# Kernel optimization log

Hardware: AMD Instinct MI355X
Metric: run time of the kernel (lower is better)

Reference implementation:

```python
import jax, jax.numpy as jnp
import numpy as np

H = 16          # num heads
DH = 64         # head size
D = H * DH      # hidden size 1024
B, S = 2, 2048


def setup_inputs() -> dict:
    key = jax.random.key(0)
    ks = jax.random.split(key, 9)
    scale = 1.0 / np.sqrt(D)
    p = {}
    p["hidden_states"] = jax.random.normal(ks[0], (B, S, D), dtype=jnp.float32)
    for i, name in enumerate(["q", "k", "v", "o"]):
        # stored so that y = x @ W + b (transpose of torch Linear weight)
        p[f"W{name}"] = jax.random.normal(ks[1 + 2 * i], (D, D), dtype=jnp.float32) * scale
        p[f"b{name}"] = jax.random.normal(ks[2 + 2 * i], (D,), dtype=jnp.float32) * 0.01
    return p


def reference(hidden_states, Wq, bq, Wk, bk, Wv, bv, Wo, bo):
    b, s, _ = hidden_states.shape
    q = hidden_states @ Wq + bq  # [B,S,D]
    k = hidden_states @ Wk + bk
    v = hidden_states @ Wv + bv
    # [B,H,S,DH]
    q = q.reshape(b, s, H, DH).transpose(0, 2, 1, 3)
    k = k.reshape(b, s, H, DH).transpose(0, 2, 1, 3)
    v = v.reshape(b, s, H, DH).transpose(0, 2, 1, 3)
    scores = jnp.einsum("bhqd,bhkd->bhqk", q, k) / np.sqrt(DH)
    causal = jnp.triu(jnp.ones((s, s), dtype=bool), k=1)  # True above diagonal -> masked
    scores = jnp.where(causal, -jnp.inf, scores)
    attn = jax.nn.softmax(scores, axis=-1)  # dropout p=0 (eval)
    ctx = jnp.einsum("bhqk,bhkd->bhqd", attn, v)
    ctx = ctx.transpose(0, 2, 1, 3).reshape(b, s, D)
    return ctx @ Wo + bo
```

## Files before the change

kernel.cpp:

```cpp
#include <hip/hip_runtime.h>


typedef _Float16 f16x8 __attribute__((ext_vector_type(8)));
typedef _Float16 f16x4 __attribute__((ext_vector_type(4)));
typedef float f32x4 __attribute__((ext_vector_type(4)));

#define GLD_LDS16(g, l)                                                        \
  __builtin_amdgcn_global_load_lds(                                            \
      (__attribute__((address_space(1))) const unsigned int*)(g),              \
      (__attribute__((address_space(3))) unsigned int*)(l), 16, 0, 0)

static constexpr int Sdim = 2048;
static constexpr int Ddim = 1024;
static constexpr int NH = 16;
static constexpr int DH = 64;
static constexpr int Mrows = 4096;

static constexpr float QSCALE = 0.125f * 1.44269504f;
static constexpr float SHIFT = 4.0f;

__global__ __launch_bounds__(256) void xcvt(const float* __restrict__ X,
                                            _Float16* __restrict__ Y) {
  size_t i = ((size_t)blockIdx.x * 256 + threadIdx.x) * 8;
  float4 f0 = *(const float4*)(X + i);
  float4 f1 = *(const float4*)(X + i + 4);
  alignas(16) _Float16 h[8] = {(_Float16)f0.x, (_Float16)f0.y, (_Float16)f0.z,
                               (_Float16)f0.w, (_Float16)f1.x, (_Float16)f1.y,
                               (_Float16)f1.z, (_Float16)f1.w};
  *(uint4*)(Y + i) = *(const uint4*)h;
}

struct WtArgs {
  const float *s0, *s1, *s2, *s3;
  _Float16 *d0, *d1, *d2, *d3;
};

__global__ __launch_bounds__(256) void wtrans(WtArgs a) {
  __shared__ _Float16 L[64 * 72];
  const int z = blockIdx.z;
  const float* src = z == 0 ? a.s0 : z == 1 ? a.s1 : z == 2 ? a.s2 : a.s3;
  _Float16* dst = z == 0 ? a.d0 : z == 1 ? a.d1 : z == 2 ? a.d2 : a.d3;
  const int k0 = blockIdx.x * 64, n0 = blockIdx.y * 64, t = threadIdx.x;
#pragma unroll
  for (int i = 0; i < 4; ++i) {
    int c = i * 256 + t;
    int row = c >> 4, cc = c & 15;
    float4 f = *(const float4*)&src[(size_t)(k0 + row) * Ddim + n0 + cc * 4];
    L[(cc * 4 + 0) * 72 + row] = (_Float16)f.x;
    L[(cc * 4 + 1) * 72 + row] = (_Float16)f.y;
    L[(cc * 4 + 2) * 72 + row] = (_Float16)f.z;
    L[(cc * 4 + 3) * 72 + row] = (_Float16)f.w;
  }
  __syncthreads();
#pragma unroll
  for (int i = 0; i < 2; ++i) {
    int c = i * 256 + t;
    int n = c >> 3, cc = c & 7;
    *(uint4*)&dst[(size_t)(n0 + n) * Ddim + k0 + cc * 8] =
        *(const uint4*)&L[n * 72 + cc * 8];
  }
}

struct GemmArgs {
  const _Float16* A;
  const _Float16 *Bt0, *Bt1, *Bt2;
  const float *b0, *b1, *b2;
  void *o0, *o1, *o2;
};

template <int MODE>
__global__ __launch_bounds__(256) void gemm128(GemmArgs g) {
  constexpr int K = 1024;
  __shared__ _Float16 As[128 * 32];
  __shared__ _Float16 Bs[128 * 32];
  const int z = blockIdx.z;
  const _Float16* A = g.A;
  const _Float16* Bt = z == 0 ? g.Bt0 : z == 1 ? g.Bt1 : g.Bt2;
  const float* bias = z == 0 ? g.b0 : z == 1 ? g.b1 : g.b2;
  void* out = z == 0 ? g.o0 : z == 1 ? g.o1 : g.o2;
  const int m0 = blockIdx.x * 128, n0 = blockIdx.y * 128;
  const int t = threadIdx.x, lane = t & 63, wv = t >> 6;
  const int wm = wv >> 1, wn = wv & 1, quad = lane >> 4, r = lane & 15;

  const int c0 = wv * 64 + lane, c1 = c0 + 256;
  const _Float16* ga0 = A + (size_t)(m0 + (c0 >> 2)) * K + (c0 & 3) * 8;
  const _Float16* ga1 = A + (size_t)(m0 + (c1 >> 2)) * K + (c1 & 3) * 8;
  const _Float16* gb0 = Bt + (size_t)(n0 + (c0 >> 2)) * K + (c0 & 3) * 8;
  const _Float16* gb1 = Bt + (size_t)(n0 + (c1 >> 2)) * K + (c1 & 3) * 8;
  char* lA0 = (char*)As + (wv * 64) * 16;
  char* lA1 = (char*)As + (256 + wv * 64) * 16;
  char* lB0 = (char*)Bs + (wv * 64) * 16;
  char* lB1 = (char*)Bs + (256 + wv * 64) * 16;

  f32x4 acc[4][4] = {};
  for (int kt = 0; kt < K; kt += 32) {
    GLD_LDS16(ga0 + kt, lA0);
    GLD_LDS16(ga1 + kt, lA1);
    GLD_LDS16(gb0 + kt, lB0);
    GLD_LDS16(gb1 + kt, lB1);
    __syncthreads();
    f16x8 af[4], bf[4];
#pragma unroll
    for (int mi = 0; mi < 4; ++mi)
      af[mi] = *(const f16x8*)&As[(wm * 64 + mi * 16 + r) * 32 + quad * 8];
#pragma unroll
    for (int ni = 0; ni < 4; ++ni)
      bf[ni] = *(const f16x8*)&Bs[(wn * 64 + ni * 16 + r) * 32 + quad * 8];
#pragma unroll
    for (int mi = 0; mi < 4; ++mi)
#pragma unroll
      for (int ni = 0; ni < 4; ++ni)
        acc[mi][ni] = __builtin_amdgcn_mfma_f32_16x16x32_f16(af[mi], bf[ni],
                                                             acc[mi][ni], 0, 0, 0);
    __syncthreads();
  }

  const float scale = (MODE == 0 && z == 0) ? QSCALE : 1.0f;
  float bv[4];
#pragma unroll
  for (int ni = 0; ni < 4; ++ni) bv[ni] = bias[n0 + wn * 64 + ni * 16 + r];
#pragma unroll
  for (int mi = 0; mi < 4; ++mi) {
#pragma unroll
    for (int ni = 0; ni < 4; ++ni) {
      const int n = n0 + wn * 64 + ni * 16 + r;
      if (MODE == 0 && z == 2) {
        alignas(8) _Float16 h4[4];
#pragma unroll
        for (int reg = 0; reg < 4; ++reg)
          h4[reg] = (_Float16)(acc[mi][ni][reg] + bv[ni]);
        const int m = m0 + wm * 64 + mi * 16 + quad * 4;
        const int b = m >> 11, s = m & 2047, h = n >> 6, dh = n & 63;
        *(uint2*)&((_Float16*)out)[((size_t)(b * NH + h) * DH + dh) * Sdim + s] =
            *(const uint2*)h4;
      } else {
#pragma unroll
        for (int reg = 0; reg < 4; ++reg) {
          const int m = m0 + wm * 64 + mi * 16 + quad * 4 + reg;
          const float v = (acc[mi][ni][reg] + bv[ni]) * scale;
          if (MODE == 0) {
            const int b = m >> 11, s = m & 2047, h = n >> 6, dh = n & 63;
            ((_Float16*)out)[(((size_t)(b * NH + h) * Sdim + s) << 6) + dh] =
                (_Float16)v;
          } else {
            ((float*)out)[(size_t)m * Ddim + n] = v;
          }
        }
      }
    }
  }
}

__global__ __launch_bounds__(256) void attn(const _Float16* __restrict__ Q,
                                            const _Float16* __restrict__ Kk,
                                            const _Float16* __restrict__ Vt,
                                            _Float16* __restrict__ ctx) {
  constexpr int LDK = 72;
  __shared__ _Float16 Ks[2][64 * LDK], Vs[2][64 * LDK], Ps[4 * 16 * LDK];
  const int id = blockIdx.x, xcd = id & 7, slot = id >> 3;
  const int x = slot & 15, bh = ((slot >> 4) << 3) | xcd;
  const int t = threadIdx.x, lane = t & 63, wv = t >> 6;
  const int quad = lane >> 4, r = lane & 15;
  const _Float16* Kg = Kk + (size_t)bh * Sdim * DH;
  const _Float16* Vg = Vt + (size_t)bh * DH * Sdim;
  _Float16* Pw = Ps + wv * 16 * LDK;
  const int b = bh >> 4, h = bh & 15;
  const int sr0 = t >> 3, sc0 = (t & 7) * 8, sr1 = (t + 256) >> 3;

#pragma unroll
  for (int pass = 0; pass < 2; ++pass) {
    const int qt = pass == 0 ? x : 31 - x;
    const int q0 = qt * 64;
    const _Float16* Qrow = Q + ((size_t)bh * Sdim + q0 + wv * 16 + r) * DH;
    const f16x8 aq0 = *(const f16x8*)(Qrow + quad * 8);
    const f16x8 aq1 = *(const f16x8*)(Qrow + 32 + quad * 8);
    const int qcol = q0 + wv * 16 + r;

    float l_i = 0.f;
    f32x4 oacc[4] = {};

    const int ntiles = qt + 1;
    uint4 ka = *(const uint4*)&Kg[(size_t)sr0 * DH + sc0];
    uint4 kb = *(const uint4*)&Kg[(size_t)sr1 * DH + sc0];
    uint4 va = *(const uint4*)&Vg[(size_t)sr0 * Sdim + sc0];
    uint4 vb = *(const uint4*)&Vg[(size_t)sr1 * Sdim + sc0];
    __syncthreads();
    *(uint4*)&Ks[0][sr0 * LDK + sc0] = ka;
    *(uint4*)&Ks[0][sr1 * LDK + sc0] = kb;
    *(uint4*)&Vs[0][sr0 * LDK + sc0] = va;
    *(uint4*)&Vs[0][sr1 * LDK + sc0] = vb;

    for (int it = 0; it < ntiles; ++it) {
      const int cur = it & 1;
      if (it + 1 < ntiles) {
        const int kvn = (it + 1) * 64;
        ka = *(const uint4*)&Kg[(size_t)(kvn + sr0) * DH + sc0];
        kb = *(const uint4*)&Kg[(size_t)(kvn + sr1) * DH + sc0];
        va = *(const uint4*)&Vg[(size_t)sr0 * Sdim + kvn + sc0];
        vb = *(const uint4*)&Vg[(size_t)sr1 * Sdim + kvn + sc0];
      }
      __syncthreads();

      f32x4 sacc[4] = {};
#pragma unroll
      for (int ks = 0; ks < 2; ++ks) {
        const f16x8 bq = ks ? aq1 : aq0;
#pragma unroll
        for (int ni = 0; ni < 4; ++ni) {
          f16x8 ak =
              *(const f16x8*)&Ks[cur][(ni * 16 + r) * LDK + ks * 32 + quad * 8];
          sacc[ni] =
              __builtin_amdgcn_mfma_f32_16x16x32_f16(ak, bq, sacc[ni], 0, 0, 0);
        }
      }

      const bool diag = (it == ntiles - 1);
      const int kvb = it * 64;
      float lp = 0.f;
#pragma unroll
      for (int ni = 0; ni < 4; ++ni) {
        alignas(8) f16x4 h4;
#pragma unroll
        for (int reg = 0; reg < 4; ++reg) {
          float sv = sacc[ni][reg];
          if (diag && (kvb + ni * 16 + quad * 4 + reg > qcol)) sv = -1e30f;
          const float p = exp2f(sv - SHIFT);
          lp += p;
          h4[reg] = (_Float16)p;
        }
        *(f16x4*)&Pw[r * LDK + ni * 16 + quad * 4] = h4;
      }
      lp += __shfl_xor(lp, 16, 64);
      lp += __shfl_xor(lp, 32, 64);
      l_i += lp;

#pragma unroll
      for (int ks = 0; ks < 2; ++ks) {
        f16x8 ap = *(const f16x8*)&Pw[r * LDK + ks * 32 + quad * 8];
#pragma unroll
        for (int ni = 0; ni < 4; ++ni) {
          f16x8 bv =
              *(const f16x8*)&Vs[cur][(ni * 16 + r) * LDK + ks * 32 + quad * 8];
          oacc[ni] =
              __builtin_amdgcn_mfma_f32_16x16x32_f16(ap, bv, oacc[ni], 0, 0, 0);
        }
      }

      if (it + 1 < ntiles) {
        const int nxt = cur ^ 1;
        *(uint4*)&Ks[nxt][sr0 * LDK + sc0] = ka;
        *(uint4*)&Ks[nxt][sr1 * LDK + sc0] = kb;
        *(uint4*)&Vs[nxt][sr0 * LDK + sc0] = va;
        *(uint4*)&Vs[nxt][sr1 * LDK + sc0] = vb;
      }
    }

#pragma unroll
    for (int reg = 0; reg < 4; ++reg) {
      const float lq = __shfl(l_i, quad * 4 + reg, 16);
      const float rl = 1.0f / lq;
      const int qrow = q0 + wv * 16 + quad * 4 + reg;
#pragma unroll
      for (int ni = 0; ni < 4; ++ni) {
        ctx[((size_t)b * Sdim + qrow) * Ddim + h * DH + ni * 16 + r] =
            (_Float16)(oacc[ni][reg] * rl);
      }
    }
  }
}

extern "C" void kernel_launch(void* const* d_in, const int* in_sizes, int n_in,
                              void* d_out, int out_size, void* d_ws,
                              size_t ws_size, hipStream_t stream) {
  const float* hid = (const float*)d_in[0];
  const float* Wq = (const float*)d_in[1];
  const float* bq = (const float*)d_in[2];
  const float* Wk = (const float*)d_in[3];
  const float* bk = (const float*)d_in[4];
  const float* Wv = (const float*)d_in[5];
  const float* bv = (const float*)d_in[6];
  const float* Wo = (const float*)d_in[7];
  const float* bo = (const float*)d_in[8];

  char* ws = (char*)d_ws;
  _Float16* Xh = (_Float16*)(ws);
  _Float16* Wqt = (_Float16*)(ws + (8ull << 20));
  _Float16* Wkt = (_Float16*)(ws + (10ull << 20));
  _Float16* Wvt = (_Float16*)(ws + (12ull << 20));
  _Float16* Wot = (_Float16*)(ws + (14ull << 20));
  _Float16* Qb = (_Float16*)(ws + (16ull << 20));
  _Float16* Kb = (_Float16*)(ws + (24ull << 20));
  _Float16* Vtb = (_Float16*)(ws + (32ull << 20));
  _Float16* ctx = Xh;

  xcvt<<<dim3(Mrows * Ddim / (256 * 8)), 256, 0, stream>>>(hid, Xh);

  WtArgs wa{Wq, Wk, Wv, Wo, Wqt, Wkt, Wvt, Wot};
  wtrans<<<dim3(16, 16, 4), 256, 0, stream>>>(wa);

  GemmArgs g1{Xh, Wqt, Wkt, Wvt, bq, bk, bv, Qb, Kb, Vtb};
  gemm128<0><<<dim3(Mrows / 128, Ddim / 128, 3), 256, 0, stream>>>(g1);

  attn<<<dim3(512), 256, 0, stream>>>(Qb, Kb, Vtb, ctx);

  GemmArgs g2{ctx, Wot, Wot, Wot, bo, bo, bo, d_out, d_out, d_out};
  gemm128<1><<<dim3(Mrows / 128, Ddim / 128, 1), 256, 0, stream>>>(g2);
}
```

Measured before the change: 193.6 us.

## Merge prep kernels, split attention into one q-tile per block with register-shuffled P

Fuses the fp16 conversion of the activations and the weight transposes into one launch, removing a kernel launch. The attention kernel now runs one query tile per block (1024 blocks instead of 512 blocks doing paired tiles) with a rebalanced tile-to-block mapping. P is passed to the PV MFMA through cross-lane shuffles in registers instead of an LDS round trip, with a transposed accumulator that allows packed output stores. The risks are extra shuffle instructions and losing the paired-tile load balancing within a block.

After: 216.2 us. 1.12x slower.

```diff
diff --git a/kernel.cpp b/kernel.cpp
--- a/kernel.cpp
+++ b/kernel.cpp
@@ -2,7 +2,6 @@
 
 
 typedef _Float16 f16x8 __attribute__((ext_vector_type(8)));
-typedef _Float16 f16x4 __attribute__((ext_vector_type(4)));
 typedef float f32x4 __attribute__((ext_vector_type(4)));
 
 #define GLD_LDS16(g, l)                                                        \
@@ -19,28 +18,29 @@
 static constexpr float QSCALE = 0.125f * 1.44269504f;
 static constexpr float SHIFT = 4.0f;
 
-__global__ __launch_bounds__(256) void xcvt(const float* __restrict__ X,
-                                            _Float16* __restrict__ Y) {
-  size_t i = ((size_t)blockIdx.x * 256 + threadIdx.x) * 8;
-  float4 f0 = *(const float4*)(X + i);
-  float4 f1 = *(const float4*)(X + i + 4);
-  alignas(16) _Float16 h[8] = {(_Float16)f0.x, (_Float16)f0.y, (_Float16)f0.z,
-                               (_Float16)f0.w, (_Float16)f1.x, (_Float16)f1.y,
-                               (_Float16)f1.z, (_Float16)f1.w};
-  *(uint4*)(Y + i) = *(const uint4*)h;
-}
-
 struct WtArgs {
   const float *s0, *s1, *s2, *s3;
   _Float16 *d0, *d1, *d2, *d3;
 };
 
-__global__ __launch_bounds__(256) void wtrans(WtArgs a) {
+__global__ __launch_bounds__(256) void prep(const float* __restrict__ X,
+                                            _Float16* __restrict__ Y, WtArgs a) {
   __shared__ _Float16 L[64 * 72];
-  const int z = blockIdx.z;
+  const int bid = blockIdx.x, t = threadIdx.x;
+  if (bid < 2048) {
+    size_t i = ((size_t)bid * 256 + t) * 8;
+    float4 f0 = *(const float4*)(X + i);
+    float4 f1 = *(const float4*)(X + i + 4);
+    alignas(16) _Float16 h[8] = {(_Float16)f0.x, (_Float16)f0.y, (_Float16)f0.z,
+                                 (_Float16)f0.w, (_Float16)f1.x, (_Float16)f1.y,
+                                 (_Float16)f1.z, (_Float16)f1.w};
+    *(uint4*)(Y + i) = *(const uint4*)h;
+    return;
+  }
+  const int w = bid - 2048, z = w >> 8, rem = w & 255;
   const float* src = z == 0 ? a.s0 : z == 1 ? a.s1 : z == 2 ? a.s2 : a.s3;
   _Float16* dst = z == 0 ? a.d0 : z == 1 ? a.d1 : z == 2 ? a.d2 : a.d3;
-  const int k0 = blockIdx.x * 64, n0 = blockIdx.y * 64, t = threadIdx.x;
+  const int k0 = (rem & 15) * 64, n0 = (rem >> 4) * 64;
 #pragma unroll
   for (int i = 0; i < 4; ++i) {
     int c = i * 256 + t;
@@ -156,116 +156,125 @@
                                             const _Float16* __restrict__ Vt,
                                             _Float16* __restrict__ ctx) {
   constexpr int LDK = 72;
-  __shared__ _Float16 Ks[2][64 * LDK], Vs[2][64 * LDK], Ps[4 * 16 * LDK];
-  const int id = blockIdx.x, xcd = id & 7, slot = id >> 3;
-  const int x = slot & 15, bh = ((slot >> 4) << 3) | xcd;
+  __shared__ _Float16 Ks[2][64 * LDK], Vs[2][64 * LDK];
+  const int id = blockIdx.x, xcd = id & 7, k = id >> 3;
+  const int b2 = (k >> 5) & 3, qi = k & 31;
+  const int gg = ((qi >> 1) + 9 * b2) & 15;
+  const int qt = (qi & 1) ? (31 - gg) : gg;
+  const int bh = xcd + 8 * b2;
   const int t = threadIdx.x, lane = t & 63, wv = t >> 6;
   const int quad = lane >> 4, r = lane & 15;
   const _Float16* Kg = Kk + (size_t)bh * Sdim * DH;
   const _Float16* Vg = Vt + (size_t)bh * DH * Sdim;
-  _Float16* Pw = Ps + wv * 16 * LDK;
+  const int q0 = qt * 64;
+
+  const _Float16* Qrow = Q + ((size_t)bh * Sdim + q0 + wv * 16 + r) * DH;
+  const f16x8 bq0 = *(const f16x8*)(Qrow + quad * 8);
+  const f16x8 bq1 = *(const f16x8*)(Qrow + 32 + quad * 8);
+
+  const int sr0 = t >> 3, sr1 = sr0 + 32, sc0 = (t & 7) * 8;
+  const _Float16* pk0 = Kg + sr0 * DH + sc0;
+  const _Float16* pk1 = Kg + sr1 * DH + sc0;
+  const _Float16* pv0 = Vg + (size_t)sr0 * Sdim + sc0;
+  const _Float16* pv1 = Vg + (size_t)sr1 * Sdim + sc0;
+
+  const int sl = ((quad & 1) << 5) + r, sh = sl + 16;
+
+  float l_i = 0.f;
+  f32x4 oaccT[4] = {};
+
+  const int ntiles = qt + 1;
+  uint4 ka = *(const uint4*)pk0, kb = *(const uint4*)pk1;
+  uint4 va = *(const uint4*)pv0, vb = *(const uint4*)pv1;
+
+  for (int it = 0; it < ntiles; ++it) {
+    const int cur = it & 1;
+    *(uint4*)&Ks[cur][sr0 * LDK + sc0] = ka;
+    *(uint4*)&Ks[cur][sr1 * LDK + sc0] = kb;
+    *(uint4*)&Vs[cur][sr0 * LDK + sc0] = va;
+    *(uint4*)&Vs[cur][sr1 * LDK + sc0] = vb;
+    __syncthreads();
+    if (it + 1 < ntiles) {
+      pk0 += 64 * DH; pk1 += 64 * DH; pv0 += 64; pv1 += 64;
+      ka = *(const uint4*)pk0; kb = *(const uint4*)pk1;
+      va = *(const uint4*)pv0; vb = *(const uint4*)pv1;
+    }
+
+    f32x4 sacc[4] = {};
+#pragma unroll
+    for (int ks = 0; ks < 2; ++ks) {
+      const f16x8 bq = ks ? bq1 : bq0;
+#pragma unroll
+      for (int ni = 0; ni < 4; ++ni) {
+        f16x8 ak =
+            *(const f16x8*)&Ks[cur][(ni * 16 + r) * LDK + ks * 32 + quad * 8];
+        sacc[ni] =
+            __builtin_amdgcn_mfma_f32_16x16x32_f16(ak, bq, sacc[ni], 0, 0, 0);
+      }
+    }
+
+    if (it == ntiles - 1) {
+      const int qloc = wv * 16 + r;
+#pragma unroll
+      for (int ni = 0; ni < 4; ++ni)
+#pragma unroll
+        for (int reg = 0; reg < 4; ++reg)
+          if (16 * ni + 4 * quad + reg > qloc) sacc[ni][reg] = -1e30f;
+    }
+    int P4x[4], P4y[4];
+    float lp = 0.f;
+#pragma unroll
+    for (int ni = 0; ni < 4; ++ni) {
+      const float p0 = exp2f(sacc[ni][0] - SHIFT);
+      const float p1 = exp2f(sacc[ni][1] - SHIFT);
+      const float p2 = exp2f(sacc[ni][2] - SHIFT);
+      const float p3 = exp2f(sacc[ni][3] - SHIFT);
+      lp += (p0 + p1) + (p2 + p3);
+      P4x[ni] = __builtin_bit_cast(int, __builtin_amdgcn_cvt_pkrtz(p0, p1));
+      P4y[ni] = __builtin_bit_cast(int, __builtin_amdgcn_cvt_pkrtz(p2, p3));
+    }
+    lp += __shfl_xor(lp, 16, 64);
+    lp += __shfl_xor(lp, 32, 64);
+    l_i += lp;
+
+#pragma unroll
+    for (int ks = 0; ks < 2; ++ks) {
+      const int ax = __shfl(P4x[2 * ks], sl, 64);
+      const int ay = __shfl(P4y[2 * ks], sl, 64);
+      const int bx = __shfl(P4x[2 * ks + 1], sl, 64);
+      const int by = __shfl(P4y[2 * ks + 1], sl, 64);
+      const int cx = __shfl(P4x[2 * ks], sh, 64);
+      const int cy = __shfl(P4y[2 * ks], sh, 64);
+      const int dx = __shfl(P4x[2 * ks + 1], sh, 64);
+      const int dy = __shfl(P4y[2 * ks + 1], sh, 64);
+      int4 bi;
+      bi.x = quad >= 2 ? bx : ax;
+      bi.y = quad >= 2 ? by : ay;
+      bi.z = quad >= 2 ? dx : cx;
+      bi.w = quad >= 2 ? dy : cy;
+      const f16x8 bp = __builtin_bit_cast(f16x8, bi);
+#pragma unroll
+      for (int ni = 0; ni < 4; ++ni) {
+        f16x8 av =
+            *(const f16x8*)&Vs[cur][(ni * 16 + r) * LDK + ks * 32 + quad * 8];
+        oaccT[ni] =
+            __builtin_amdgcn_mfma_f32_16x16x32_f16(av, bp, oaccT[ni], 0, 0, 0);
+      }
+    }
+  }
+
   const int b = bh >> 4, h = bh & 15;
-  const int sr0 = t >> 3, sc0 = (t & 7) * 8, sr1 = (t + 256) >> 3;
-
-#pragma unroll
-  for (int pass = 0; pass < 2; ++pass) {
-    const int qt = pass == 0 ? x : 31 - x;
-    const int q0 = qt * 64;
-    const _Float16* Qrow = Q + ((size_t)bh * Sdim + q0 + wv * 16 + r) * DH;
-    const f16x8 aq0 = *(const f16x8*)(Qrow + quad * 8);
-    const f16x8 aq1 = *(const f16x8*)(Qrow + 32 + quad * 8);
-    const int qcol = q0 + wv * 16 + r;
-
-    float l_i = 0.f;
-    f32x4 oacc[4] = {};
-
-    const int ntiles = qt + 1;
-    uint4 ka = *(const uint4*)&Kg[(size_t)sr0 * DH + sc0];
-    uint4 kb = *(const uint4*)&Kg[(size_t)sr1 * DH + sc0];
-    uint4 va = *(const uint4*)&Vg[(size_t)sr0 * Sdim + sc0];
-    uint4 vb = *(const uint4*)&Vg[(size_t)sr1 * Sdim + sc0];
-    __syncthreads();
-    *(uint4*)&Ks[0][sr0 * LDK + sc0] = ka;
-    *(uint4*)&Ks[0][sr1 * LDK + sc0] = kb;
-    *(uint4*)&Vs[0][sr0 * LDK + sc0] = va;
-    *(uint4*)&Vs[0][sr1 * LDK + sc0] = vb;
-
-    for (int it = 0; it < ntiles; ++it) {
-      const int cur = it & 1;
-      if (it + 1 < ntiles) {
-        const int kvn = (it + 1) * 64;
-        ka = *(const uint4*)&Kg[(size_t)(kvn + sr0) * DH + sc0];
-        kb = *(const uint4*)&Kg[(size_t)(kvn + sr1) * DH + sc0];
-        va = *(const uint4*)&Vg[(size_t)sr0 * Sdim + kvn + sc0];
-        vb = *(const uint4*)&Vg[(size_t)sr1 * Sdim + kvn + sc0];
-      }
-      __syncthreads();
-
-      f32x4 sacc[4] = {};
-#pragma unroll
-      for (int ks = 0; ks < 2; ++ks) {
-        const f16x8 bq = ks ? aq1 : aq0;
-#pragma unroll
-        for (int ni = 0; ni < 4; ++ni) {
-          f16x8 ak =
-              *(const f16x8*)&Ks[cur][(ni * 16 + r) * LDK + ks * 32 + quad * 8];
-          sacc[ni] =
-              __builtin_amdgcn_mfma_f32_16x16x32_f16(ak, bq, sacc[ni], 0, 0, 0);
-        }
-      }
-
-      const bool diag = (it == ntiles - 1);
-      const int kvb = it * 64;
-      float lp = 0.f;
-#pragma unroll
-      for (int ni = 0; ni < 4; ++ni) {
-        alignas(8) f16x4 h4;
-#pragma unroll
-        for (int reg = 0; reg < 4; ++reg) {
-          float sv = sacc[ni][reg];
-          if (diag && (kvb + ni * 16 + quad * 4 + reg > qcol)) sv = -1e30f;
-          const float p = exp2f(sv - SHIFT);
-          lp += p;
-          h4[reg] = (_Float16)p;
-        }
-        *(f16x4*)&Pw[r * LDK + ni * 16 + quad * 4] = h4;
-      }
-      lp += __shfl_xor(lp, 16, 64);
-      lp += __shfl_xor(lp, 32, 64);
-      l_i += lp;
-
-#pragma unroll
-      for (int ks = 0; ks < 2; ++ks) {
-        f16x8 ap = *(const f16x8*)&Pw[r * LDK + ks * 32 + quad * 8];
-#pragma unroll
-        for (int ni = 0; ni < 4; ++ni) {
-          f16x8 bv =
-              *(const f16x8*)&Vs[cur][(ni * 16 + r) * LDK + ks * 32 + quad * 8];
-          oacc[ni] =
-              __builtin_amdgcn_mfma_f32_16x16x32_f16(ap, bv, oacc[ni], 0, 0, 0);
-        }
-      }
-
-      if (it + 1 < ntiles) {
-        const int nxt = cur ^ 1;
-        *(uint4*)&Ks[nxt][sr0 * LDK + sc0] = ka;
-        *(uint4*)&Ks[nxt][sr1 * LDK + sc0] = kb;
-        *(uint4*)&Vs[nxt][sr0 * LDK + sc0] = va;
-        *(uint4*)&Vs[nxt][sr1 * LDK + sc0] = vb;
-      }
-    }
-
-#pragma unroll
-    for (int reg = 0; reg < 4; ++reg) {
-      const float lq = __shfl(l_i, quad * 4 + reg, 16);
-      const float rl = 1.0f / lq;
-      const int qrow = q0 + wv * 16 + quad * 4 + reg;
-#pragma unroll
-      for (int ni = 0; ni < 4; ++ni) {
-        ctx[((size_t)b * Sdim + qrow) * Ddim + h * DH + ni * 16 + r] =
-            (_Float16)(oacc[ni][reg] * rl);
-      }
-    }
+  const float rl = 1.0f / l_i;
+  _Float16* crow =
+      ctx + ((size_t)b * Sdim + q0 + wv * 16 + r) * Ddim + h * DH + quad * 4;
+#pragma unroll
+  for (int ni = 0; ni < 4; ++ni) {
+    int2 st;
+    st.x = __builtin_bit_cast(
+        int, __builtin_amdgcn_cvt_pkrtz(oaccT[ni][0] * rl, oaccT[ni][1] * rl));
+    st.y = __builtin_bit_cast(
+        int, __builtin_amdgcn_cvt_pkrtz(oaccT[ni][2] * rl, oaccT[ni][3] * rl));
+    *(int2*)(crow + ni * 16) = st;
   }
 }
 
@@ -293,15 +302,13 @@
   _Float16* Vtb = (_Float16*)(ws + (32ull << 20));
   _Float16* ctx = Xh;
 
-  xcvt<<<dim3(Mrows * Ddim / (256 * 8)), 256, 0, stream>>>(hid, Xh);
-
   WtArgs wa{Wq, Wk, Wv, Wo, Wqt, Wkt, Wvt, Wot};
-  wtrans<<<dim3(16, 16, 4), 256, 0, stream>>>(wa);
+  prep<<<dim3(2048 + 1024), 256, 0, stream>>>(hid, Xh, wa);
 
   GemmArgs g1{Xh, Wqt, Wkt, Wvt, bq, bk, bv, Qb, Kb, Vtb};
   gemm128<0><<<dim3(Mrows / 128, Ddim / 128, 3), 256, 0, stream>>>(g1);
 
-  attn<<<dim3(512), 256, 0, stream>>>(Qb, Kb, Vtb, ctx);
+  attn<<<dim3(1024), 256, 0, stream>>>(Qb, Kb, Vtb, ctx);
 
   GemmArgs g2{ctx, Wot, Wot, Wot, bo, bo, bo, d_out, d_out, d_out};
   gemm128<1><<<dim3(Mrows / 128, Ddim / 128, 1), 256, 0, stream>>>(g2);
```
